# Optimization experiments

Hardware: AMD Instinct MI355X
Metric: run time of the kernel (lower is better)

## Reference

```python
import jax, jax.numpy as jnp
import numpy as np

B, P = 65536, 22  # sets, max players per freeze frame
IN, HID, OUT = 6, 64, 128


def setup_inputs() -> dict:
    key = jax.random.key(0)
    k0, k1, k2, k3, k4, k5 = jax.random.split(key, 6)
    pitch = jnp.array([120.0, 80.0], dtype=jnp.float32)
    player_locs = jax.random.uniform(k0, (B, P, 2), dtype=jnp.float32) * pitch
    actor_locs = jax.random.uniform(k1, (B, 2), dtype=jnp.float32) * pitch
    # teammate / keeper flags in {0,1}
    flags = jax.random.randint(k2, (B, P, 2), 0, 2).astype(jnp.float32)
    # validity mask: 0 -> player skipped (simulates ragged / missing entries)
    mask = jax.random.randint(k3, (B, P), 0, 2).astype(jnp.int32)
    W1 = jax.random.normal(k4, (IN, HID), dtype=jnp.float32) / np.sqrt(IN)
    b1 = jnp.zeros((HID,), dtype=jnp.float32)
    W2 = jax.random.normal(k5, (HID, OUT), dtype=jnp.float32) / np.sqrt(HID)
    b2 = jnp.zeros((OUT,), dtype=jnp.float32)
    return {"player_locs": player_locs, "actor_locs": actor_locs, "flags": flags,
            "mask": mask, "W1": W1, "b1": b1, "W2": W2, "b2": b2}


def reference(player_locs, actor_locs, flags, mask, W1, b1, W2, b2):
    # per-player features relative to the actor: [dx, dy, dist, angle, teammate, keeper]
    dxy = player_locs - actor_locs[:, None, :]                 # [B,P,2]
    dist = jnp.sqrt(jnp.sum(dxy * dxy, axis=-1, keepdims=True))  # [B,P,1]
    angle = jnp.arctan2(dxy[..., 1:2], dxy[..., 0:1])            # [B,P,1]
    feats = jnp.concatenate([dxy, dist, angle, flags], axis=-1)  # [B,P,6]
    # PlayerMLP: Linear -> ReLU -> Linear
    h = jax.nn.relu(jnp.einsum('bpi,ih->bph', feats, W1) + b1)   # [B,P,64]
    emb = jnp.einsum('bph,ho->bpo', h, W2) + b2                  # [B,P,128]
    # masked mean over valid players; empty sets yield zeros (sum is 0)
    m = mask.astype(emb.dtype)[..., None]                        # [B,P,1]
    cnt = jnp.sum(m, axis=1)                                     # [B,1]
    pooled = jnp.sum(emb * m, axis=1) / jnp.maximum(cnt, 1.0)    # [B,128]
    return pooled
```

## Files before the change

kernel.cpp:

```cpp
#include <hip/hip_runtime.h>
#include <math.h>

#define PMAX 22
#define HID 64
#define OUTD 128
#define SETS_PER_WAVE 8
#define WAVES_PER_BLOCK 4
#define ROWS (PMAX * SETS_PER_WAVE)

__device__ __forceinline__ void wave_lds_sync() {
    asm volatile("s_waitcnt lgkmcnt(0)" ::: "memory");
    __builtin_amdgcn_wave_barrier();
}

__global__ __launch_bounds__(256) void set_encoder_kernel(
    const float* __restrict__ player_locs,
    const float* __restrict__ actor_locs,
    const float* __restrict__ flags,
    const int*   __restrict__ mask,
    const float* __restrict__ W1,
    const float* __restrict__ b1,
    const float* __restrict__ W2,
    const float* __restrict__ b2,
    float* __restrict__ out)
{
    __shared__ float feats[WAVES_PER_BLOCK][ROWS][8];
    __shared__ float hbars[WAVES_PER_BLOCK][HID][SETS_PER_WAVE];

    const int tid  = threadIdx.x;
    const int lane = tid & 63;
    const int wave = tid >> 6;

    const int wave_id = blockIdx.x * WAVES_PER_BLOCK + wave;
    const int set0    = wave_id * SETS_PER_WAVE;
    const int row0    = set0 * PMAX;

    const float w10 = W1[0 * HID + lane];
    const float w11 = W1[1 * HID + lane];
    const float w12 = W1[2 * HID + lane];
    const float w13 = W1[3 * HID + lane];
    const float w14 = W1[4 * HID + lane];
    const float w15 = W1[5 * HID + lane];
    const float b1l = b1[lane];

    unsigned long long bm[3];
#pragma unroll
    for (int i = 0; i < 3; ++i) {
        const int idx  = lane + 64 * i;
        const int ridx = idx < ROWS ? idx : ROWS - 1;
        float2 pl = ((const float2*)player_locs)[row0 + ridx];
        float2 fl = ((const float2*)flags)[row0 + ridx];
        int    m  = mask[row0 + ridx];
        const int s = ridx / PMAX;
        float2 ac = ((const float2*)actor_locs)[set0 + s];
        float dx = pl.x - ac.x;
        float dy = pl.y - ac.y;
        float dist = sqrtf(dx * dx + dy * dy);
        float ang  = atan2f(dy, dx);
        bm[i] = __ballot((idx < ROWS) && (m != 0));
        if (idx < ROWS) {
            float4* fr = (float4*)&feats[wave][ridx][0];
            fr[0] = make_float4(dx, dy, dist, ang);
            fr[1] = make_float4(fl.x, fl.y, 0.0f, 0.0f);
        }
    }
    wave_lds_sync();

    unsigned nonempty = 0;
#pragma unroll
    for (int s = 0; s < SETS_PER_WAVE; ++s) {
        const int start = PMAX * s;
        const int w = start >> 6, r = start & 63;
        unsigned long long lo = bm[w] >> r;
        if (r > 64 - PMAX) lo |= bm[w + 1] << (64 - r);
        unsigned bits = (unsigned)lo & 0x3FFFFFu;

        const int cnt = __builtin_popcount(bits);
        if (bits) nonempty |= (1u << s);

        const float* fb = &feats[wave][start][0];
        float acc = 0.0f;
        unsigned bb = bits;
        while (bb) {
            const int p = __builtin_ctz(bb);
            bb &= bb - 1;
            const float* fp = fb + (p << 3);
            float4 fA = *(const float4*)fp;
            float2 fB = *(const float2*)(fp + 4);
            float t0 = fmaf(fA.x, w10, b1l);
            t0 = fmaf(fA.y, w11, t0);
            t0 = fmaf(fA.z, w12, t0);
            float t1 = fA.w * w13;
            t1 = fmaf(fB.x, w14, t1);
            t1 = fmaf(fB.y, w15, t1);
            acc += fmaxf(t0 + t1, 0.0f);
        }
        const float scale = 1.0f / fmaxf((float)cnt, 1.0f);
        hbars[wave][lane][s] = acc * scale;
    }
    wave_lds_sync();

    float a0[SETS_PER_WAVE], a1[SETS_PER_WAVE];
#pragma unroll
    for (int s = 0; s < SETS_PER_WAVE; ++s) { a0[s] = 0.0f; a1[s] = 0.0f; }

    const float2* w2p = (const float2*)W2;
#pragma unroll 8
    for (int k = 0; k < HID; ++k) {
        float2 w2v = w2p[k * 64 + lane];
        float4 h0  = *(const float4*)&hbars[wave][k][0];
        float4 h1  = *(const float4*)&hbars[wave][k][4];
        a0[0] = fmaf(h0.x, w2v.x, a0[0]); a1[0] = fmaf(h0.x, w2v.y, a1[0]);
        a0[1] = fmaf(h0.y, w2v.x, a0[1]); a1[1] = fmaf(h0.y, w2v.y, a1[1]);
        a0[2] = fmaf(h0.z, w2v.x, a0[2]); a1[2] = fmaf(h0.z, w2v.y, a1[2]);
        a0[3] = fmaf(h0.w, w2v.x, a0[3]); a1[3] = fmaf(h0.w, w2v.y, a1[3]);
        a0[4] = fmaf(h1.x, w2v.x, a0[4]); a1[4] = fmaf(h1.x, w2v.y, a1[4]);
        a0[5] = fmaf(h1.y, w2v.x, a0[5]); a1[5] = fmaf(h1.y, w2v.y, a1[5]);
        a0[6] = fmaf(h1.z, w2v.x, a0[6]); a1[6] = fmaf(h1.z, w2v.y, a1[6]);
        a0[7] = fmaf(h1.w, w2v.x, a0[7]); a1[7] = fmaf(h1.w, w2v.y, a1[7]);
    }

    const float2 b2v = *(const float2*)&b2[2 * lane];
#pragma unroll
    for (int s = 0; s < SETS_PER_WAVE; ++s) {
        const float f = (nonempty >> s) & 1u ? 1.0f : 0.0f;
        float2 o;
        o.x = a0[s] + f * b2v.x;
        o.y = a1[s] + f * b2v.y;
        ((float2*)out)[(size_t)(set0 + s) * (OUTD / 2) + lane] = o;
    }
}

extern "C" void kernel_launch(void* const* d_in, const int* in_sizes, int n_in,
                              void* d_out, int out_size, void* d_ws, size_t ws_size,
                              hipStream_t stream) {
    const float* player_locs = (const float*)d_in[0];
    const float* actor_locs  = (const float*)d_in[1];
    const float* flags       = (const float*)d_in[2];
    const int*   mask        = (const int*)d_in[3];
    const float* W1          = (const float*)d_in[4];
    const float* b1          = (const float*)d_in[5];
    const float* W2          = (const float*)d_in[6];
    const float* b2          = (const float*)d_in[7];
    float*       out         = (float*)d_out;

    const int B = in_sizes[0] / (PMAX * 2);
    const int sets_per_block = WAVES_PER_BLOCK * SETS_PER_WAVE;
    const int grid = (B + sets_per_block - 1) / sets_per_block;

    hipLaunchKernelGGL(set_encoder_kernel, dim3(grid), dim3(256), 0, stream,
                       player_locs, actor_locs, flags, mask, W1, b1, W2, b2, out);
}
```

Before: 120.6 us.

## Replace LDS staging with register-resident features and readlane broadcasts

Removes the shared-memory buffers for per-player features and pooled hidden vectors. Features are kept in registers, two sets per 64-lane group, and broadcast to all lanes with v_readlane. The second layer also reads hidden values through readlane and software-prefetches the next W2 row. This drops LDS traffic and the wave syncs, but adds many scalar readlane instructions and SGPR-to-VGPR moves, and the feature load is regrouped into four 44-lane passes that leave 20 lanes idle.

```diff
diff --git a/kernel.cpp b/kernel.cpp
--- a/kernel.cpp
+++ b/kernel.cpp
@@ -6,11 +6,9 @@
 #define OUTD 128
 #define SETS_PER_WAVE 8
 #define WAVES_PER_BLOCK 4
-#define ROWS (PMAX * SETS_PER_WAVE)
 
-__device__ __forceinline__ void wave_lds_sync() {
-    asm volatile("s_waitcnt lgkmcnt(0)" ::: "memory");
-    __builtin_amdgcn_wave_barrier();
+__device__ __forceinline__ float rl(float v, int l) {
+    return __int_as_float(__builtin_amdgcn_readlane(__float_as_int(v), l));
 }
 
 __global__ __launch_bounds__(256) void set_encoder_kernel(
@@ -24,16 +22,12 @@
     const float* __restrict__ b2,
     float* __restrict__ out)
 {
-    __shared__ float feats[WAVES_PER_BLOCK][ROWS][8];
-    __shared__ float hbars[WAVES_PER_BLOCK][HID][SETS_PER_WAVE];
-
     const int tid  = threadIdx.x;
     const int lane = tid & 63;
     const int wave = tid >> 6;
 
     const int wave_id = blockIdx.x * WAVES_PER_BLOCK + wave;
     const int set0    = wave_id * SETS_PER_WAVE;
-    const int row0    = set0 * PMAX;
 
     const float w10 = W1[0 * HID + lane];
     const float w11 = W1[1 * HID + lane];
@@ -43,81 +37,86 @@
     const float w15 = W1[5 * HID + lane];
     const float b1l = b1[lane];
 
-    unsigned long long bm[3];
+    float fr[4][6];
+    unsigned long long bm[4];
 #pragma unroll
-    for (int i = 0; i < 3; ++i) {
-        const int idx  = lane + 64 * i;
-        const int ridx = idx < ROWS ? idx : ROWS - 1;
-        float2 pl = ((const float2*)player_locs)[row0 + ridx];
-        float2 fl = ((const float2*)flags)[row0 + ridx];
-        int    m  = mask[row0 + ridx];
-        const int s = ridx / PMAX;
-        float2 ac = ((const float2*)actor_locs)[set0 + s];
+    for (int g = 0; g < 4; ++g) {
+        const int lidx = lane < 2 * PMAX ? lane : 2 * PMAX - 1;
+        const int grow = (set0 + 2 * g) * PMAX + lidx;
+        float2 pl = ((const float2*)player_locs)[grow];
+        float2 fl = ((const float2*)flags)[grow];
+        int    m  = mask[grow];
+        const int sl = 2 * g + (lidx >= PMAX ? 1 : 0);
+        float2 ac = ((const float2*)actor_locs)[set0 + sl];
         float dx = pl.x - ac.x;
         float dy = pl.y - ac.y;
-        float dist = sqrtf(dx * dx + dy * dy);
-        float ang  = atan2f(dy, dx);
-        bm[i] = __ballot((idx < ROWS) && (m != 0));
-        if (idx < ROWS) {
-            float4* fr = (float4*)&feats[wave][ridx][0];
-            fr[0] = make_float4(dx, dy, dist, ang);
-            fr[1] = make_float4(fl.x, fl.y, 0.0f, 0.0f);
-        }
+        fr[g][0] = dx;
+        fr[g][1] = dy;
+        fr[g][2] = sqrtf(dx * dx + dy * dy);
+        fr[g][3] = atan2f(dy, dx);
+        fr[g][4] = fl.x;
+        fr[g][5] = fl.y;
+        bm[g] = __ballot((lane < 2 * PMAX) && (m != 0));
     }
-    wave_lds_sync();
 
+    float hs[SETS_PER_WAVE];
     unsigned nonempty = 0;
 #pragma unroll
     for (int s = 0; s < SETS_PER_WAVE; ++s) {
-        const int start = PMAX * s;
-        const int w = start >> 6, r = start & 63;
-        unsigned long long lo = bm[w] >> r;
-        if (r > 64 - PMAX) lo |= bm[w + 1] << (64 - r);
-        unsigned bits = (unsigned)lo & 0x3FFFFFu;
-
+        const int g    = s >> 1;
+        const int base = (s & 1) * PMAX;
+        unsigned bits = (unsigned)(bm[g] >> base) & 0x3FFFFFu;
         const int cnt = __builtin_popcount(bits);
         if (bits) nonempty |= (1u << s);
-
-        const float* fb = &feats[wave][start][0];
         float acc = 0.0f;
         unsigned bb = bits;
         while (bb) {
             const int p = __builtin_ctz(bb);
             bb &= bb - 1;
-            const float* fp = fb + (p << 3);
-            float4 fA = *(const float4*)fp;
-            float2 fB = *(const float2*)(fp + 4);
-            float t0 = fmaf(fA.x, w10, b1l);
-            t0 = fmaf(fA.y, w11, t0);
-            t0 = fmaf(fA.z, w12, t0);
-            float t1 = fA.w * w13;
-            t1 = fmaf(fB.x, w14, t1);
-            t1 = fmaf(fB.y, w15, t1);
+            const int src = base + p;
+            float f0 = rl(fr[g][0], src);
+            float f1 = rl(fr[g][1], src);
+            float f2 = rl(fr[g][2], src);
+            float f3 = rl(fr[g][3], src);
+            float f4 = rl(fr[g][4], src);
+            float f5 = rl(fr[g][5], src);
+            float t0 = fmaf(f0, w10, b1l);
+            t0 = fmaf(f1, w11, t0);
+            t0 = fmaf(f2, w12, t0);
+            float t1 = f3 * w13;
+            t1 = fmaf(f4, w14, t1);
+            t1 = fmaf(f5, w15, t1);
             acc += fmaxf(t0 + t1, 0.0f);
         }
-        const float scale = 1.0f / fmaxf((float)cnt, 1.0f);
-        hbars[wave][lane][s] = acc * scale;
+        hs[s] = acc * (1.0f / fmaxf((float)cnt, 1.0f));
     }
-    wave_lds_sync();
 
     float a0[SETS_PER_WAVE], a1[SETS_PER_WAVE];
 #pragma unroll
     for (int s = 0; s < SETS_PER_WAVE; ++s) { a0[s] = 0.0f; a1[s] = 0.0f; }
 
     const float2* w2p = (const float2*)W2;
+    float2 w2v = w2p[lane];
 #pragma unroll 8
     for (int k = 0; k < HID; ++k) {
-        float2 w2v = w2p[k * 64 + lane];
-        float4 h0  = *(const float4*)&hbars[wave][k][0];
-        float4 h1  = *(const float4*)&hbars[wave][k][4];
-        a0[0] = fmaf(h0.x, w2v.x, a0[0]); a1[0] = fmaf(h0.x, w2v.y, a1[0]);
-        a0[1] = fmaf(h0.y, w2v.x, a0[1]); a1[1] = fmaf(h0.y, w2v.y, a1[1]);
-        a0[2] = fmaf(h0.z, w2v.x, a0[2]); a1[2] = fmaf(h0.z, w2v.y, a1[2]);
-        a0[3] = fmaf(h0.w, w2v.x, a0[3]); a1[3] = fmaf(h0.w, w2v.y, a1[3]);
-        a0[4] = fmaf(h1.x, w2v.x, a0[4]); a1[4] = fmaf(h1.x, w2v.y, a1[4]);
-        a0[5] = fmaf(h1.y, w2v.x, a0[5]); a1[5] = fmaf(h1.y, w2v.y, a1[5]);
-        a0[6] = fmaf(h1.z, w2v.x, a0[6]); a1[6] = fmaf(h1.z, w2v.y, a1[6]);
-        a0[7] = fmaf(h1.w, w2v.x, a0[7]); a1[7] = fmaf(h1.w, w2v.y, a1[7]);
+        const float2 cur = w2v;
+        w2v = w2p[(((k + 1) & 63) * 64) + lane];
+        const float h0 = rl(hs[0], k);
+        const float h1 = rl(hs[1], k);
+        const float h2 = rl(hs[2], k);
+        const float h3 = rl(hs[3], k);
+        const float h4 = rl(hs[4], k);
+        const float h5 = rl(hs[5], k);
+        const float h6 = rl(hs[6], k);
+        const float h7 = rl(hs[7], k);
+        a0[0] = fmaf(h0, cur.x, a0[0]); a1[0] = fmaf(h0, cur.y, a1[0]);
+        a0[1] = fmaf(h1, cur.x, a0[1]); a1[1] = fmaf(h1, cur.y, a1[1]);
+        a0[2] = fmaf(h2, cur.x, a0[2]); a1[2] = fmaf(h2, cur.y, a1[2]);
+        a0[3] = fmaf(h3, cur.x, a0[3]); a1[3] = fmaf(h3, cur.y, a1[3]);
+        a0[4] = fmaf(h4, cur.x, a0[4]); a1[4] = fmaf(h4, cur.y, a1[4]);
+        a0[5] = fmaf(h5, cur.x, a0[5]); a1[5] = fmaf(h5, cur.y, a1[5]);
+        a0[6] = fmaf(h6, cur.x, a0[6]); a1[6] = fmaf(h6, cur.y, a1[6]);
+        a0[7] = fmaf(h7, cur.x, a0[7]); a1[7] = fmaf(h7, cur.y, a1[7]);
     }
 
     const float2 b2v = *(const float2*)&b2[2 * lane];
```

New measurement: 139.0 us. 15.3% more time.
